# Optimization experiments

Hardware: AMD Instinct MI355X
Metric: run time of the kernel (lower is better)

Reference implementation:

```python
import jax, jax.numpy as jnp
import numpy as np

# Sizes (match input_specs)
B = 50                 # number of CRN graphs in the batch
NS_PER, NR_PER = 2000, 4000
N_S, N_R = B * NS_PER, B * NR_PER   # 100k species, 200k reactions total
E = 1_000_000          # bipartite edges
D = 128                # d_model
L = 2                  # n_layers
N_TYPES, P_DIM = 16, 8
MAX_SPECIES_IDX = 2000


def setup_inputs() -> dict:
    key = jax.random.key(0)
    ks = jax.random.split(key, 12)
    inp = {
        "species_indices": jax.random.randint(ks[0], (N_S,), 0, MAX_SPECIES_IDX, dtype=jnp.int32),
        "is_external": jax.random.randint(ks[1], (N_S,), 0, 2, dtype=jnp.int32),
        "propensity_type_ids": jax.random.randint(ks[2], (N_R,), 0, N_TYPES, dtype=jnp.int32),
        "propensity_params": jax.random.normal(ks[3], (N_R, P_DIM), dtype=jnp.float32),
        "edge_species": jax.random.randint(ks[4], (E,), 0, N_S, dtype=jnp.int32),
        "edge_reaction": jax.random.randint(ks[5], (E,), 0, N_R, dtype=jnp.int32),
        # contiguous per-graph segment ids (graphs are equal-sized)
        "species_batch": jnp.repeat(jnp.arange(B, dtype=jnp.int32), NS_PER),
        "reaction_batch": jnp.repeat(jnp.arange(B, dtype=jnp.int32), NR_PER),
        # learned parameters
        "species_table": jax.random.normal(ks[6], (MAX_SPECIES_IDX, D), dtype=jnp.float32) * 0.02,
        "external_table": jax.random.normal(ks[7], (2, D), dtype=jnp.float32) * 0.02,
        "type_table": jax.random.normal(ks[8], (N_TYPES, D), dtype=jnp.float32) * 0.02,
        "W_param": jax.random.normal(ks[9], (P_DIM, D), dtype=jnp.float32) * 0.1,
        "b_param": jnp.zeros((D,), dtype=jnp.float32),
        # per-layer message-passing weights: concat([h, msg]) -> d
        "Wr": jax.random.normal(ks[10], (L, 2 * D, D), dtype=jnp.float32) * 0.05,
        "br": jnp.zeros((L, D), dtype=jnp.float32),
        "Ws": jax.random.normal(ks[11], (L, 2 * D, D), dtype=jnp.float32) * 0.05,
        "bs": jnp.zeros((L, D), dtype=jnp.float32),
    }
    return inp


def reference(species_indices, is_external, propensity_type_ids, propensity_params,
              edge_species, edge_reaction, species_batch, reaction_batch,
              species_table, external_table, type_table, W_param, b_param,
              Wr, br, Ws, bs):
    # Initial embeddings
    h_s = species_table[species_indices] + external_table[is_external]          # (N_S, D)
    h_r = type_table[propensity_type_ids] + propensity_params @ W_param + b_param  # (N_R, D)

    n_s, n_r = h_s.shape[0], h_r.shape[0]
    # Alternating bipartite sum message passing (SumMessagePassingLayer)
    for l in range(Wr.shape[0]):
        m_r = jax.ops.segment_sum(h_s[edge_species], edge_reaction, num_segments=n_r)
        h_r = jax.nn.relu(jnp.concatenate([h_r, m_r], axis=-1) @ Wr[l] + br[l])
        m_s = jax.ops.segment_sum(h_r[edge_reaction], edge_species, num_segments=n_s)
        h_s = jax.nn.relu(jnp.concatenate([h_s, m_s], axis=-1) @ Ws[l] + bs[l])

    # Segment-mean pooling per graph (index_add then divide by counts)
    pooled_s = jax.ops.segment_sum(h_s, species_batch, num_segments=B) / float(NS_PER)
    pooled_r = jax.ops.segment_sum(h_r, reaction_batch, num_segments=B) / float(NR_PER)
    context = jnp.concatenate([pooled_s, pooled_r], axis=-1)  # (B, 2D); dropout p=0 -> identity
    return context
```

## Files before the change

kernel.cpp:

```cpp
#include <hip/hip_runtime.h>
#include <stdint.h>

#define NS 100000
#define NR 200000
#define EE 1000000
#define DD 128
#define NB 50
#define NSP 2000
#define NRP 4000
#define BSH 10
#define NBR 196
#define NBS 98
#define CHUNK 8192

typedef short bf16x8 __attribute__((ext_vector_type(8)));
typedef float f32x4 __attribute__((ext_vector_type(4)));
typedef float f32x2 __attribute__((ext_vector_type(2)));
typedef unsigned u32x4 __attribute__((ext_vector_type(4)));
typedef unsigned u32x2 __attribute__((ext_vector_type(2)));

__device__ __forceinline__ unsigned short f2bf(float f){
  unsigned u = __float_as_uint(f);
  u = (u + 0x7FFFu + ((u >> 16) & 1u)) >> 16;
  return (unsigned short)u;
}
__device__ __forceinline__ float bf2f(unsigned short s){
  return __uint_as_float(((unsigned)s) << 16);
}
__device__ __forceinline__ unsigned packbf(float a, float b){
  return (unsigned)f2bf(a) | ((unsigned)f2bf(b) << 16);
}
__device__ __forceinline__ float bflo(unsigned p){ return __uint_as_float(p << 16); }
__device__ __forceinline__ float bfhi(unsigned p){ return __uint_as_float(p & 0xFFFF0000u); }

__device__ __forceinline__ u32x2 packf8(const float* v){
  u32x2 r;
  unsigned w = __builtin_amdgcn_cvt_pk_fp8_f32(v[0], v[1], 0u, false);
  r.x = __builtin_amdgcn_cvt_pk_fp8_f32(v[2], v[3], w, true);
  w = __builtin_amdgcn_cvt_pk_fp8_f32(v[4], v[5], 0u, false);
  r.y = __builtin_amdgcn_cvt_pk_fp8_f32(v[6], v[7], w, true);
  return r;
}
__device__ __forceinline__ void acc8f8(float* a, u32x2 p){
  f32x2 f;
  f = __builtin_amdgcn_cvt_pk_f32_fp8(p.x, false); a[0]+=f.x; a[1]+=f.y;
  f = __builtin_amdgcn_cvt_pk_f32_fp8(p.x, true);  a[2]+=f.x; a[3]+=f.y;
  f = __builtin_amdgcn_cvt_pk_f32_fp8(p.y, false); a[4]+=f.x; a[5]+=f.y;
  f = __builtin_amdgcn_cvt_pk_f32_fp8(p.y, true);  a[6]+=f.x; a[7]+=f.y;
}

__global__ void pack_w(const float* __restrict__ Wr, const float* __restrict__ Ws,
                       unsigned short* __restrict__ Wp){
  int g = blockIdx.x*256 + threadIdx.x;
  if (g >= 4*32768) return;
  int j = g & 7; int rest = g >> 3;
  int lane = rest & 63; rest >>= 6;
  int ks = rest & 7; rest >>= 3;
  int ct = rest & 7; int mat = rest >> 3;
  int k  = ks*32 + (lane >> 4)*8 + j;
  int cc = ct*16 + (lane & 15);
  const float* src = (mat < 2) ? (Wr + (size_t)mat*256*DD) : (Ws + (size_t)(mat-2)*256*DD);
  Wp[g] = f2bf(src[(size_t)k*DD + cc]);
}

__global__ __launch_bounds__(256) void init_all(const int* __restrict__ si, const int* __restrict__ ext,
        const int* __restrict__ tid, const float* __restrict__ pp,
        const float* __restrict__ st, const float* __restrict__ et, const float* __restrict__ tt,
        const float* __restrict__ Wpar, const float* __restrict__ bpar,
        unsigned short* __restrict__ hs, unsigned short* __restrict__ hr,
        unsigned char* __restrict__ f8S, unsigned char* __restrict__ f8R){
  int g = blockIdx.x*256 + threadIdx.x;
  int row = g >> 4, colb = (g & 15) * 8;
  float v[8];
  if (row < NS){
    const float* a = st + (size_t)si[row]*DD + colb;
    const float* b = et + (size_t)ext[row]*DD + colb;
    float4 x0 = ((const float4*)a)[0], x1 = ((const float4*)a)[1];
    float4 y0 = ((const float4*)b)[0], y1 = ((const float4*)b)[1];
    v[0]=x0.x+y0.x; v[1]=x0.y+y0.y; v[2]=x0.z+y0.z; v[3]=x0.w+y0.w;
    v[4]=x1.x+y1.x; v[5]=x1.y+y1.y; v[6]=x1.z+y1.z; v[7]=x1.w+y1.w;
    u32x4 o;
    o.x = packbf(v[0],v[1]); o.y = packbf(v[2],v[3]);
    o.z = packbf(v[4],v[5]); o.w = packbf(v[6],v[7]);
    *(u32x4*)(hs + (size_t)row*DD + colb) = o;
    *(u32x2*)(f8S + (size_t)row*DD + colb) = packf8(v);
  } else {
    int r = row - NS;
    const float* tb = tt + (size_t)tid[r]*DD + colb;
    float4 a0 = ((const float4*)tb)[0], a1 = ((const float4*)tb)[1];
    float4 b0 = ((const float4*)(bpar+colb))[0], b1 = ((const float4*)(bpar+colb))[1];
    a0.x += b0.x; a0.y += b0.y; a0.z += b0.z; a0.w += b0.w;
    a1.x += b1.x; a1.y += b1.y; a1.z += b1.z; a1.w += b1.w;
    const float* pr = pp + (size_t)r*8;
    float4 p0 = ((const float4*)pr)[0], p1 = ((const float4*)pr)[1];
    float w[8] = {p0.x,p0.y,p0.z,p0.w,p1.x,p1.y,p1.z,p1.w};
    #pragma unroll
    for (int p = 0; p < 8; p++){
      float4 w0 = ((const float4*)(Wpar + p*DD + colb))[0];
      float4 w1 = ((const float4*)(Wpar + p*DD + colb))[1];
      a0.x += w[p]*w0.x; a0.y += w[p]*w0.y; a0.z += w[p]*w0.z; a0.w += w[p]*w0.w;
      a1.x += w[p]*w1.x; a1.y += w[p]*w1.y; a1.z += w[p]*w1.z; a1.w += w[p]*w1.w;
    }
    v[0]=a0.x; v[1]=a0.y; v[2]=a0.z; v[3]=a0.w;
    v[4]=a1.x; v[5]=a1.y; v[6]=a1.z; v[7]=a1.w;
    u32x4 o;
    o.x = packbf(v[0],v[1]); o.y = packbf(v[2],v[3]);
    o.z = packbf(v[4],v[5]); o.w = packbf(v[6],v[7]);
    *(u32x4*)(hr + (size_t)r*DD + colb) = o;
    *(u32x2*)(f8R + (size_t)r*DD + colb) = packf8(v);
  }
}

__global__ __launch_bounds__(256) void bucket_hist(const int* __restrict__ er, const int* __restrict__ es,
                                                   int* __restrict__ gcnt){
  __shared__ int cnt[NBR + NBS];
  int t = threadIdx.x;
  for (int j = t; j < NBR + NBS; j += 256) cnt[j] = 0;
  __syncthreads();
  long i0 = (long)blockIdx.x * 2048;
  for (int j = t; j < 2048; j += 256){
    long i = i0 + j;
    if (i < EE){
      atomicAdd(&cnt[er[i] >> BSH], 1);
      atomicAdd(&cnt[NBR + (es[i] >> BSH)], 1);
    }
  }
  __syncthreads();
  for (int j = t; j < NBR + NBS; j += 256)
    if (cnt[j]) atomicAdd(&gcnt[j], cnt[j]);
}

__global__ __launch_bounds__(256) void bucket_scan(const int* __restrict__ gcnt,
        int* __restrict__ bktOffR, int* __restrict__ bktOffS,
        int* __restrict__ gCurR, int* __restrict__ gCurS){
  __shared__ int a[256];
  int t = threadIdx.x;
  int own = (t < NBR) ? gcnt[t] : 0;
  a[t] = own; __syncthreads();
  for (int d = 1; d < 256; d <<= 1){
    int x = (t >= d) ? a[t-d] : 0;
    __syncthreads(); a[t] += x; __syncthreads();
  }
  if (t < NBR){ int v = a[t] - own; bktOffR[t] = v; gCurR[t] = v; }
  if (t == 0) bktOffR[NBR] = EE;
  __syncthreads();
  own = (t < NBS) ? gcnt[NBR + t] : 0;
  a[t] = own; __syncthreads();
  for (int d = 1; d < 256; d <<= 1){
    int x = (t >= d) ? a[t-d] : 0;
    __syncthreads(); a[t] += x; __syncthreads();
  }
  if (t < NBS){ int v = a[t] - own; bktOffS[t] = v; gCurS[t] = v; }
  if (t == 0) bktOffS[NBS] = EE;
}

__global__ __launch_bounds__(256) void bin_edges(const int* __restrict__ er, const int* __restrict__ es,
        int* __restrict__ gCurR, int* __restrict__ gCurS,
        unsigned* __restrict__ recR, unsigned* __restrict__ recS){
  __shared__ unsigned stage[CHUNK];
  __shared__ unsigned char stageb[CHUNK];
  __shared__ int cnt[256], scn[256], pref[256], gbase[256], lcur[256];
  int t = threadIdx.x;
  int side = blockIdx.y;
  const int* dest = side ? es : er;
  const int* srca = side ? er : es;
  int* gCur = side ? gCurS : gCurR;
  unsigned* rec = side ? recS : recR;
  int nbkt = side ? NBS : NBR;
  long i0 = (long)blockIdx.x * CHUNK;
  int n = (EE - i0 < CHUNK) ? (int)(EE - i0) : CHUNK;
  cnt[t] = 0;
  __syncthreads();
  for (int j = t; j < n; j += 256)
    atomicAdd(&cnt[dest[i0 + j] >> BSH], 1);
  __syncthreads();
  scn[t] = cnt[t];
  __syncthreads();
  for (int d = 1; d < 256; d <<= 1){
    int x = (t >= d) ? scn[t-d] : 0;
    __syncthreads(); scn[t] += x; __syncthreads();
  }
  pref[t] = scn[t] - cnt[t];
  lcur[t] = scn[t] - cnt[t];
  if (t < nbkt && cnt[t] > 0) gbase[t] = atomicAdd(&gCur[t], cnt[t]);
  __syncthreads();
  for (int j = t; j < n; j += 256){
    int d = dest[i0 + j];
    int s = srca[i0 + j];
    int b = d >> BSH;
    int p = atomicAdd(&lcur[b], 1);
    stage[p] = ((unsigned)(d - (b << BSH)) << 18) | (unsigned)s;
    stageb[p] = (unsigned char)b;
  }
  __syncthreads();
  for (int e = t; e < n; e += 256){
    int b = stageb[e];
    rec[gbase[b] + (e - pref[b])] = stage[e];
  }
}

__global__ __launch_bounds__(256) void build_csr(const unsigned* __restrict__ recR, const unsigned* __restrict__ recS,
        const int* __restrict__ bktOffR, const int* __restrict__ bktOffS,
        int* __restrict__ csrR, int* __restrict__ csrS,
        int* __restrict__ offsR, int* __restrict__ offsS){
  __shared__ int hist[1024], pref[1024], cur[1024], ws[256];
  int t = threadIdx.x;
  int bb = blockIdx.x;
  const unsigned* rec; const int* bktOff; int* csr; int* offs; int N;
  if (bb < NBR){ rec = recR; bktOff = bktOffR; csr = csrR; offs = offsR; N = NR; }
  else { bb -= NBR; rec = recS; bktOff = bktOffS; csr = csrS; offs = offsS; N = NS; }
  int d0 = bb << BSH;
  int base = bktOff[bb], cnt_ = bktOff[bb+1] - base;
  #pragma unroll
  for (int j = 0; j < 4; j++) hist[t*4+j] = 0;
  __syncthreads();
  for (int e = t; e < cnt_; e += 256)
    atomicAdd(&hist[rec[base + e] >> 18], 1);
  __syncthreads();
  int s = 0, h[4];
  #pragma unroll
  for (int j = 0; j < 4; j++){ h[j] = hist[t*4+j]; s += h[j]; }
  ws[t] = s;
  __syncthreads();
  for (int d = 1; d < 256; d <<= 1){
    int x = (t >= d) ? ws[t-d] : 0;
    __syncthreads(); ws[t] += x; __syncthreads();
  }
  int run = ws[t] - s;
  #pragma unroll
  for (int j = 0; j < 4; j++){ pref[t*4+j] = run; cur[t*4+j] = base + run; run += h[j]; }
  __syncthreads();
  int DPB = N - d0; if (DPB > 1024) DPB = 1024;
  #pragma unroll
  for (int j = 0; j < 4; j++){
    int i = t*4 + j;
    if (i < DPB) offs[d0 + i] = base + pref[i];
  }
  if (t == 0 && d0 + DPB == N) offs[N] = EE;
  __syncthreads();
  for (int e = t; e < cnt_; e += 256){
    unsigned r = rec[base + e];
    int pos = atomicAdd(&cur[r >> 18], 1);
    csr[pos] = (int)(r & 0x3FFFFu);
  }
}

__global__ __launch_bounds__(256) void fused_layer(
        const unsigned char* __restrict__ g8,
        const unsigned short* __restrict__ hself,
        const int* __restrict__ offs, const int* __restrict__ csr,
        const unsigned short* __restrict__ Wp, const float* __restrict__ bias,
        unsigned short* __restrict__ hout, unsigned char* __restrict__ hout8)
{
  __shared__ unsigned short msgT[32*DD];
  int t = threadIdx.x;
  int lane = t & 63;
  int w = t >> 6;
  int quad = lane >> 4, rlo = lane & 15;
  int row0 = blockIdx.x * 32;

  {
    int lr1 = w*8 + quad, lr2 = lr1 + 4;
    int r1 = row0 + lr1, r2 = row0 + lr2;
    int k1 = offs[r1], e1 = offs[r1+1];
    int k2 = offs[r2], e2 = offs[r2+1];
    float xa[8] = {0,0,0,0,0,0,0,0};
    float ya[8] = {0,0,0,0,0,0,0,0};
    while (k1 + 2 <= e1 && k2 + 2 <= e2){
      int sA = csr[k1], sB = csr[k1+1], sC = csr[k2], sD = csr[k2+1];
      u32x2 pA = *(const u32x2*)(g8 + (size_t)sA*DD + rlo*8);
      u32x2 pB = *(const u32x2*)(g8 + (size_t)sB*DD + rlo*8);
      u32x2 pC = *(const u32x2*)(g8 + (size_t)sC*DD + rlo*8);
      u32x2 pD = *(const u32x2*)(g8 + (size_t)sD*DD + rlo*8);
      acc8f8(xa, pA); acc8f8(xa, pB); acc8f8(ya, pC); acc8f8(ya, pD);
      k1 += 2; k2 += 2;
    }
    while (k1 + 2 <= e1){
      int sA = csr[k1], sB = csr[k1+1];
      u32x2 pA = *(const u32x2*)(g8 + (size_t)sA*DD + rlo*8);
      u32x2 pB = *(const u32x2*)(g8 + (size_t)sB*DD + rlo*8);
      acc8f8(xa, pA); acc8f8(xa, pB);
      k1 += 2;
    }
    while (k2 + 2 <= e2){
      int sC = csr[k2], sD = csr[k2+1];
      u32x2 pC = *(const u32x2*)(g8 + (size_t)sC*DD + rlo*8);
      u32x2 pD = *(const u32x2*)(g8 + (size_t)sD*DD + rlo*8);
      acc8f8(ya, pC); acc8f8(ya, pD);
      k2 += 2;
    }
    if (k1 < e1){ u32x2 p = *(const u32x2*)(g8 + (size_t)csr[k1]*DD + rlo*8); acc8f8(xa, p); }
    if (k2 < e2){ u32x2 p = *(const u32x2*)(g8 + (size_t)csr[k2]*DD + rlo*8); acc8f8(ya, p); }
    u32x4 o1, o2;
    o1.x = packbf(xa[0],xa[1]); o1.y = packbf(xa[2],xa[3]);
    o1.z = packbf(xa[4],xa[5]); o1.w = packbf(xa[6],xa[7]);
    o2.x = packbf(ya[0],ya[1]); o2.y = packbf(ya[2],ya[3]);
    o2.z = packbf(ya[4],ya[5]); o2.w = packbf(ya[6],ya[7]);
    *(u32x4*)(msgT + lr1*DD + ((rlo ^ (lr1 & 7)) * 8)) = o1;
    *(u32x4*)(msgT + lr2*DD + ((rlo ^ (lr2 & 7)) * 8)) = o2;
  }
  __syncthreads();

  int ct0 = w * 2;
  bf16x8 wf[16];
  #pragma unroll
  for (int ks = 0; ks < 8; ks++){
    wf[ks*2+0] = *(const bf16x8*)(Wp + (size_t)(((ct0+0)*8 + ks)*64 + lane) * 8);
    wf[ks*2+1] = *(const bf16x8*)(Wp + (size_t)(((ct0+1)*8 + ks)*64 + lane) * 8);
  }
  bf16x8 Hb0[4], Hb1[4];
  #pragma unroll
  for (int ks = 0; ks < 4; ks++){
    int kloc = ks*32 + quad*8;
    Hb0[ks] = *(const bf16x8*)(hself + (size_t)(row0 + rlo) * DD + kloc);
    Hb1[ks] = *(const bf16x8*)(hself + (size_t)(row0 + 16 + rlo) * DD + kloc);
  }
  bf16x8 Mb0[4], Mb1[4];
  #pragma unroll
  for (int ks2 = 0; ks2 < 4; ks2++){
    int c8 = ks2*4 + quad;
    int lr0 = rlo, lr1 = 16 + rlo;
    Mb0[ks2] = *(const bf16x8*)(msgT + lr0*DD + ((c8 ^ (lr0 & 7)) * 8));
    Mb1[ks2] = *(const bf16x8*)(msgT + lr1*DD + ((c8 ^ (lr1 & 7)) * 8));
  }

  f32x4 acc[2][2];
  #pragma unroll
  for (int i = 0; i < 2; i++)
    #pragma unroll
    for (int j = 0; j < 2; j++){ f32x4 z = {0.f,0.f,0.f,0.f}; acc[i][j] = z; }

  #pragma unroll
  for (int ks = 0; ks < 4; ks++){
    acc[0][0] = __builtin_amdgcn_mfma_f32_16x16x32_bf16(wf[ks*2+0], Hb0[ks], acc[0][0], 0, 0, 0);
    acc[0][1] = __builtin_amdgcn_mfma_f32_16x16x32_bf16(wf[ks*2+1], Hb0[ks], acc[0][1], 0, 0, 0);
    acc[1][0] = __builtin_amdgcn_mfma_f32_16x16x32_bf16(wf[ks*2+0], Hb1[ks], acc[1][0], 0, 0, 0);
    acc[1][1] = __builtin_amdgcn_mfma_f32_16x16x32_bf16(wf[ks*2+1], Hb1[ks], acc[1][1], 0, 0, 0);
  }
  #pragma unroll
  for (int ks2 = 0; ks2 < 4; ks2++){
    int ks = 4 + ks2;
    acc[0][0] = __builtin_amdgcn_mfma_f32_16x16x32_bf16(wf[ks*2+0], Mb0[ks2], acc[0][0], 0, 0, 0);
    acc[0][1] = __builtin_amdgcn_mfma_f32_16x16x32_bf16(wf[ks*2+1], Mb0[ks2], acc[0][1], 0, 0, 0);
    acc[1][0] = __builtin_amdgcn_mfma_f32_16x16x32_bf16(wf[ks*2+0], Mb1[ks2], acc[1][0], 0, 0, 0);
    acc[1][1] = __builtin_amdgcn_mfma_f32_16x16x32_bf16(wf[ks*2+1], Mb1[ks2], acc[1][1], 0, 0, 0);
  }

  #pragma unroll
  for (int c = 0; c < 2; c++){
    float4 bv = *(const float4*)(bias + (ct0+c)*16 + quad*4);
    #pragma unroll
    for (int rb = 0; rb < 2; rb++){
      int row = row0 + rb*16 + rlo;
      float v0 = acc[rb][c][0] + bv.x;
      float v1 = acc[rb][c][1] + bv.y;
      float v2 = acc[rb][c][2] + bv.z;
      float v3 = acc[rb][c][3] + bv.w;
      v0 = v0 > 0.f ? v0 : 0.f;
      v1 = v1 > 0.f ? v1 : 0.f;
      v2 = v2 > 0.f ? v2 : 0.f;
      v3 = v3 > 0.f ? v3 : 0.f;
      u32x2 o; o.x = packbf(v0, v1); o.y = packbf(v2, v3);
      *(u32x2*)(hout + (size_t)row*DD + (ct0+c)*16 + quad*4) = o;
      unsigned w8 = __builtin_amdgcn_cvt_pk_fp8_f32(v0, v1, 0u, false);
      w8 = __builtin_amdgcn_cvt_pk_fp8_f32(v2, v3, w8, true);
      *(unsigned*)(hout8 + (size_t)row*DD + (ct0+c)*16 + quad*4) = w8;
    }
  }
}

__global__ __launch_bounds__(256) void pool(const unsigned short* __restrict__ hs,
        const unsigned short* __restrict__ hr, float* __restrict__ out){
  __shared__ float red[16][128];
  int b = blockIdx.x, part = blockIdx.y;
  int t = threadIdx.x;
  int rg = t >> 4, sub = t & 15;
  const unsigned short* src; int row0, outoff; float scale;
  if (part < 4){ src = hs; row0 = b*NSP + part*500; outoff = b*256; scale = 1.f/NSP; }
  else { src = hr; row0 = b*NRP + (part-4)*500; outoff = b*256 + 128; scale = 1.f/NRP; }
  float a0=0,a1=0,a2=0,a3=0,a4=0,a5=0,a6=0,a7=0;
  for (int r = rg; r < 500; r += 16){
    u32x4 p = *(const u32x4*)(src + (size_t)(row0+r)*DD + sub*8);
    a0 += bflo(p.x); a1 += bfhi(p.x);
    a2 += bflo(p.y); a3 += bfhi(p.y);
    a4 += bflo(p.z); a5 += bfhi(p.z);
    a6 += bflo(p.w); a7 += bfhi(p.w);
  }
  float* rr = &red[rg][sub*8];
  rr[0]=a0; rr[1]=a1; rr[2]=a2; rr[3]=a3; rr[4]=a4; rr[5]=a5; rr[6]=a6; rr[7]=a7;
  __syncthreads();
  if (t < 128){
    float s = 0.f;
    #pragma unroll
    for (int g = 0; g < 16; g++) s += red[g][t];
    atomicAdd(&out[outoff + t], s * scale);
  }
}

extern "C" void kernel_launch(void* const* d_in, const int* in_sizes, int n_in,
                              void* d_out, int out_size, void* d_ws, size_t ws_size,
                              hipStream_t stream)
{
  const int*   si   = (const int*)d_in[0];
  const int*   ext  = (const int*)d_in[1];
  const int*   tid  = (const int*)d_in[2];
  const float* pp   = (const float*)d_in[3];
  const int*   es   = (const int*)d_in[4];
  const int*   er   = (const int*)d_in[5];
  const float* st   = (const float*)d_in[8];
  const float* et   = (const float*)d_in[9];
  const float* tt   = (const float*)d_in[10];
  const float* Wpar = (const float*)d_in[11];
  const float* bpar = (const float*)d_in[12];
  const float* Wr   = (const float*)d_in[13];
  const float* br   = (const float*)d_in[14];
  const float* Ws   = (const float*)d_in[15];
  const float* bs   = (const float*)d_in[16];
  float* out = (float*)d_out;

  char* basep = (char*)d_ws; size_t off = 0;
  auto alloc = [&](size_t bytes)->char*{
    char* r = basep + off; off = (off + bytes + 255) & ~(size_t)255; return r;
  };
  unsigned short* hs0 = (unsigned short*)alloc((size_t)NS*DD*2);
  unsigned short* hs1 = (unsigned short*)alloc((size_t)NS*DD*2);
  unsigned short* hr0 = (unsigned short*)alloc((size_t)NR*DD*2);
  unsigned short* hr1 = (unsigned short*)alloc((size_t)NR*DD*2);
  unsigned char*  f8S = (unsigned char*)alloc((size_t)NS*DD);
  unsigned char*  f8R = (unsigned char*)alloc((size_t)NR*DD);
  unsigned short* Wp  = (unsigned short*)alloc((size_t)4*32768*2);
  int* offsR = (int*)alloc((size_t)(NR+1)*4);
  int* offsS = (int*)alloc((size_t)(NS+1)*4);
  int* csrR  = (int*)alloc((size_t)EE*4);
  int* csrS  = (int*)alloc((size_t)EE*4);
  int* gcnt   = (int*)alloc(2048);
  int* bktOffR= (int*)alloc(2048);
  int* bktOffS= (int*)alloc(2048);
  int* gCurR  = (int*)alloc(2048);
  int* gCurS  = (int*)alloc(2048);
  unsigned* recR = (unsigned*)hs1;
  unsigned* recS = (unsigned*)hr1;

  hipMemsetAsync(gcnt, 0, 2048, stream);
  hipMemsetAsync(d_out, 0, (size_t)out_size*4, stream);

  pack_w<<<512, 256, 0, stream>>>(Wr, Ws, Wp);
  init_all<<<(NS+NR)*16/256, 256, 0, stream>>>(si, ext, tid, pp, st, et, tt, Wpar, bpar,
                                               hs0, hr0, f8S, f8R);

  bucket_hist<<<(EE + 2047)/2048, 256, 0, stream>>>(er, es, gcnt);
  bucket_scan<<<1, 256, 0, stream>>>(gcnt, bktOffR, bktOffS, gCurR, gCurS);
  bin_edges<<<dim3((EE + CHUNK - 1)/CHUNK, 2), 256, 0, stream>>>(er, es, gCurR, gCurS, recR, recS);
  build_csr<<<NBR + NBS, 256, 0, stream>>>(recR, recS, bktOffR, bktOffS, csrR, csrS, offsR, offsS);

  fused_layer<<<NR/32, 256, 0, stream>>>(f8S, hr0, offsR, csrR, Wp + (size_t)0*32768, br + (size_t)0*DD, hr1, f8R);
  fused_layer<<<NS/32, 256, 0, stream>>>(f8R, hs0, offsS, csrS, Wp + (size_t)2*32768, bs + (size_t)0*DD, hs1, f8S);
  fused_layer<<<NR/32, 256, 0, stream>>>(f8S, hr1, offsR, csrR, Wp + (size_t)1*32768, br + (size_t)1*DD, hr0, f8R);
  fused_layer<<<NS/32, 256, 0, stream>>>(f8R, hs1, offsS, csrS, Wp + (size_t)3*32768, bs + (size_t)1*DD, hs0, f8S);

  pool<<<dim3(NB, 12), 256, 0, stream>>>(hs0, hr0, out);
}
```

Measured before the change: 531.6 us.

## Load-balance gather across block edges with LDS float atomics and prefetch

The gather phase of the fused layer stops assigning one 16-lane group per destination row. Instead the block's total edge range is split evenly across 16 groups, and each group accumulates runs belonging to the same destination into a float LDS buffer with atomics. CSR records now keep the local destination bits, so the group knows when it crosses a row boundary. The loop also software-prefetches the next four records and their FP8 gathers. This targets imbalance from varying row degrees and adds memory-level parallelism, at the cost of LDS atomics, a zeroing pass and a larger float message buffer converted to bf16 on read.

```diff
diff --git a/kernel.cpp b/kernel.cpp
--- a/kernel.cpp
+++ b/kernel.cpp
@@ -12,6 +12,7 @@
 #define NBR 196
 #define NBS 98
 #define CHUNK 8192
+#define MSTR 132
 
 typedef short bf16x8 __attribute__((ext_vector_type(8)));
 typedef float f32x4 __attribute__((ext_vector_type(4)));
@@ -32,6 +33,13 @@
 }
 __device__ __forceinline__ float bflo(unsigned p){ return __uint_as_float(p << 16); }
 __device__ __forceinline__ float bfhi(unsigned p){ return __uint_as_float(p & 0xFFFF0000u); }
+
+__device__ __forceinline__ bf16x8 pack8(float4 a, float4 b){
+  union { bf16x8 v; unsigned u[4]; } r;
+  r.u[0] = packbf(a.x, a.y); r.u[1] = packbf(a.z, a.w);
+  r.u[2] = packbf(b.x, b.y); r.u[3] = packbf(b.z, b.w);
+  return r.v;
+}
 
 __device__ __forceinline__ u32x2 packf8(const float* v){
   u32x2 r;
@@ -201,12 +209,12 @@
 
 __global__ __launch_bounds__(256) void build_csr(const unsigned* __restrict__ recR, const unsigned* __restrict__ recS,
         const int* __restrict__ bktOffR, const int* __restrict__ bktOffS,
-        int* __restrict__ csrR, int* __restrict__ csrS,
+        unsigned* __restrict__ csrR, unsigned* __restrict__ csrS,
         int* __restrict__ offsR, int* __restrict__ offsS){
   __shared__ int hist[1024], pref[1024], cur[1024], ws[256];
   int t = threadIdx.x;
   int bb = blockIdx.x;
-  const unsigned* rec; const int* bktOff; int* csr; int* offs; int N;
+  const unsigned* rec; const int* bktOff; unsigned* csr; int* offs; int N;
   if (bb < NBR){ rec = recR; bktOff = bktOffR; csr = csrR; offs = offsR; N = NR; }
   else { bb -= NBR; rec = recS; bktOff = bktOffS; csr = csrS; offs = offsS; N = NS; }
   int d0 = bb << BSH;
@@ -241,63 +249,88 @@
   for (int e = t; e < cnt_; e += 256){
     unsigned r = rec[base + e];
     int pos = atomicAdd(&cur[r >> 18], 1);
-    csr[pos] = (int)(r & 0x3FFFFu);
+    csr[pos] = r;
   }
 }
 
 __global__ __launch_bounds__(256) void fused_layer(
         const unsigned char* __restrict__ g8,
         const unsigned short* __restrict__ hself,
-        const int* __restrict__ offs, const int* __restrict__ csr,
+        const int* __restrict__ offs, const unsigned* __restrict__ csr,
         const unsigned short* __restrict__ Wp, const float* __restrict__ bias,
         unsigned short* __restrict__ hout, unsigned char* __restrict__ hout8)
 {
-  __shared__ unsigned short msgT[32*DD];
+  __shared__ float msg[32*MSTR];
   int t = threadIdx.x;
   int lane = t & 63;
   int w = t >> 6;
   int quad = lane >> 4, rlo = lane & 15;
   int row0 = blockIdx.x * 32;
 
+  for (int i = t; i < 32*MSTR; i += 256) msg[i] = 0.f;
+  __syncthreads();
+
   {
-    int lr1 = w*8 + quad, lr2 = lr1 + 4;
-    int r1 = row0 + lr1, r2 = row0 + lr2;
-    int k1 = offs[r1], e1 = offs[r1+1];
-    int k2 = offs[r2], e2 = offs[r2+1];
-    float xa[8] = {0,0,0,0,0,0,0,0};
-    float ya[8] = {0,0,0,0,0,0,0,0};
-    while (k1 + 2 <= e1 && k2 + 2 <= e2){
-      int sA = csr[k1], sB = csr[k1+1], sC = csr[k2], sD = csr[k2+1];
-      u32x2 pA = *(const u32x2*)(g8 + (size_t)sA*DD + rlo*8);
-      u32x2 pB = *(const u32x2*)(g8 + (size_t)sB*DD + rlo*8);
-      u32x2 pC = *(const u32x2*)(g8 + (size_t)sC*DD + rlo*8);
-      u32x2 pD = *(const u32x2*)(g8 + (size_t)sD*DD + rlo*8);
-      acc8f8(xa, pA); acc8f8(xa, pB); acc8f8(ya, pC); acc8f8(ya, pD);
-      k1 += 2; k2 += 2;
+    int eb = offs[row0], ee = offs[row0+32];
+    int tot = ee - eb;
+    int per = (tot + 15) >> 4;
+    int qid = w*4 + quad;
+    int k  = eb + qid*per;  if (k > ee) k = ee;
+    int ke = k + per;       if (ke > ee) ke = ee;
+    float a[8] = {0,0,0,0,0,0,0,0};
+    int cur = -1;
+    if (k < ke){
+      unsigned rc[4]; u32x2 pv[4];
+      #pragma unroll
+      for (int i = 0; i < 4; i++){
+        int kk = (k + i < ke) ? (k + i) : (ke - 1);
+        rc[i] = csr[kk];
+      }
+      #pragma unroll
+      for (int i = 0; i < 4; i++)
+        pv[i] = *(const u32x2*)(g8 + (size_t)(rc[i] & 0x3FFFF)*DD + rlo*8);
+      while (k < ke){
+        unsigned rc2[4]; u32x2 pv2[4];
+        int kn = k + 4;
+        #pragma unroll
+        for (int i = 0; i < 4; i++){
+          int kk = (kn + i < ke) ? (kn + i) : (ke - 1);
+          rc2[i] = csr[kk];
+        }
+        #pragma unroll
+        for (int i = 0; i < 4; i++)
+          pv2[i] = *(const u32x2*)(g8 + (size_t)(rc2[i] & 0x3FFFF)*DD + rlo*8);
+        #pragma unroll
+        for (int i = 0; i < 4; i++){
+          if (k + i < ke){
+            int dl = (int)((rc[i] >> 18) & 31);
+            if (dl != cur){
+              if (cur >= 0){
+                float* mp = msg + cur*MSTR + rlo*8;
+                atomicAdd(mp+0,a[0]); atomicAdd(mp+1,a[1]);
+                atomicAdd(mp+2,a[2]); atomicAdd(mp+3,a[3]);
+                atomicAdd(mp+4,a[4]); atomicAdd(mp+5,a[5]);
+                atomicAdd(mp+6,a[6]); atomicAdd(mp+7,a[7]);
+                #pragma unroll
+                for (int z = 0; z < 8; z++) a[z] = 0.f;
+              }
+              cur = dl;
+            }
+            acc8f8(a, pv[i]);
+          }
+        }
+        #pragma unroll
+        for (int i = 0; i < 4; i++){ rc[i] = rc2[i]; pv[i] = pv2[i]; }
+        k = kn;
+      }
     }
-    while (k1 + 2 <= e1){
-      int sA = csr[k1], sB = csr[k1+1];
-      u32x2 pA = *(const u32x2*)(g8 + (size_t)sA*DD + rlo*8);
-      u32x2 pB = *(const u32x2*)(g8 + (size_t)sB*DD + rlo*8);
-      acc8f8(xa, pA); acc8f8(xa, pB);
-      k1 += 2;
+    if (cur >= 0){
+      float* mp = msg + cur*MSTR + rlo*8;
+      atomicAdd(mp+0,a[0]); atomicAdd(mp+1,a[1]);
+      atomicAdd(mp+2,a[2]); atomicAdd(mp+3,a[3]);
+      atomicAdd(mp+4,a[4]); atomicAdd(mp+5,a[5]);
+      atomicAdd(mp+6,a[6]); atomicAdd(mp+7,a[7]);
     }
-    while (k2 + 2 <= e2){
-      int sC = csr[k2], sD = csr[k2+1];
-      u32x2 pC = *(const u32x2*)(g8 + (size_t)sC*DD + rlo*8);
-      u32x2 pD = *(const u32x2*)(g8 + (size_t)sD*DD + rlo*8);
-      acc8f8(ya, pC); acc8f8(ya, pD);
-      k2 += 2;
-    }
-    if (k1 < e1){ u32x2 p = *(const u32x2*)(g8 + (size_t)csr[k1]*DD + rlo*8); acc8f8(xa, p); }
-    if (k2 < e2){ u32x2 p = *(const u32x2*)(g8 + (size_t)csr[k2]*DD + rlo*8); acc8f8(ya, p); }
-    u32x4 o1, o2;
-    o1.x = packbf(xa[0],xa[1]); o1.y = packbf(xa[2],xa[3]);
-    o1.z = packbf(xa[4],xa[5]); o1.w = packbf(xa[6],xa[7]);
-    o2.x = packbf(ya[0],ya[1]); o2.y = packbf(ya[2],ya[3]);
-    o2.z = packbf(ya[4],ya[5]); o2.w = packbf(ya[6],ya[7]);
-    *(u32x4*)(msgT + lr1*DD + ((rlo ^ (lr1 & 7)) * 8)) = o1;
-    *(u32x4*)(msgT + lr2*DD + ((rlo ^ (lr2 & 7)) * 8)) = o2;
   }
   __syncthreads();
 
@@ -319,9 +352,10 @@
   #pragma unroll
   for (int ks2 = 0; ks2 < 4; ks2++){
     int c8 = ks2*4 + quad;
-    int lr0 = rlo, lr1 = 16 + rlo;
-    Mb0[ks2] = *(const bf16x8*)(msgT + lr0*DD + ((c8 ^ (lr0 & 7)) * 8));
-    Mb1[ks2] = *(const bf16x8*)(msgT + lr1*DD + ((c8 ^ (lr1 & 7)) * 8));
+    const float* p0 = msg + rlo*MSTR + c8*8;
+    const float* p1 = msg + (16+rlo)*MSTR + c8*8;
+    Mb0[ks2] = pack8(((const float4*)p0)[0], ((const float4*)p0)[1]);
+    Mb1[ks2] = pack8(((const float4*)p1)[0], ((const float4*)p1)[1]);
   }
 
   f32x4 acc[2][2];
@@ -431,8 +465,8 @@
   unsigned short* Wp  = (unsigned short*)alloc((size_t)4*32768*2);
   int* offsR = (int*)alloc((size_t)(NR+1)*4);
   int* offsS = (int*)alloc((size_t)(NS+1)*4);
-  int* csrR  = (int*)alloc((size_t)EE*4);
-  int* csrS  = (int*)alloc((size_t)EE*4);
+  unsigned* csrR = (unsigned*)alloc((size_t)EE*4);
+  unsigned* csrS = (unsigned*)alloc((size_t)EE*4);
   int* gcnt   = (int*)alloc(2048);
   int* bktOffR= (int*)alloc(2048);
   int* bktOffS= (int*)alloc(2048);
```

Measured after the change: 845.7 us. 1.59x slower.
